# Kernel optimization log

Measured on AMD Instinct MI355X. Metric: run time of the kernel, lower is better.

The kernel has to match this reference:

```python
import jax, jax.numpy as jnp
import numpy as np
from jax.scipy.special import ndtr, logsumexp

K = 2  # top-k experts (init kwarg k=2)


def setup_inputs() -> dict:
    key = jax.random.key(0)
    k1, k2, k3, k4 = jax.random.split(key, 4)
    B, D, E = 131072, 1024, 64
    x_flat = jax.random.normal(k1, (B, D), jnp.float32)
    # Original inits w_gate/w_noise to zeros; use small random weights so
    # top-k routing is non-degenerate for correctness testing.
    w_gate = jax.random.normal(k2, (D, E), jnp.float32) * 0.02
    w_noise = jax.random.normal(k3, (D, E), jnp.float32) * 0.02
    eps = jax.random.normal(k4, (B, E), jnp.float32)  # reified torch.randn_like
    return {"x_flat": x_flat, "w_gate": w_gate, "w_noise": w_noise, "eps": eps}


def _cv_squared(v):
    # torch .var() is unbiased (ddof=1)
    return jnp.var(v, ddof=1) / (jnp.mean(v) ** 2 + 1e-10)


def reference(x_flat, w_gate, w_noise, eps):
    B = x_flat.shape[0]
    clean_logits = x_flat @ w_gate                                  # [B, E]
    noise_stddev = jax.nn.softplus(x_flat @ w_noise) + 0.01         # [B, E]
    logits = clean_logits + eps * noise_stddev                      # noisy logits (training)

    top_vals, top_idx = jax.lax.top_k(logits, K + 1)                # [B, K+1], sorted desc
    top_k_gates = jax.nn.softmax(top_vals[:, :K], axis=-1)          # [B, K]
    gates = jnp.zeros_like(logits).at[jnp.arange(B)[:, None], top_idx[:, :K]].set(top_k_gates)

    # _prob_in_top_k load estimate (noisy gating, k < num_experts, training)
    thr_if_in = top_vals[:, K:K + 1]                                # (k+1)-th largest
    thr_if_out = top_vals[:, K - 1:K]                               # k-th largest
    is_in = logits > thr_if_in
    prob_if_in = ndtr((clean_logits - thr_if_in) / noise_stddev)
    prob_if_out = ndtr((clean_logits - thr_if_out) / noise_stddev)
    load = jnp.where(is_in, prob_if_in, prob_if_out).sum(0)         # [E]

    importance = gates.sum(0)                                       # [E]
    z_loss = logsumexp(logits, axis=-1).mean()                      # log(sum(exp)).mean()
    load_balancing = _cv_squared(importance) + _cv_squared(load) + z_loss
    return gates, load, logits, load_balancing, importance
```

## Files before the change

kernel.cpp:

```cpp
#include <hip/hip_runtime.h>
#include <math.h>

#define B_ROWS 131072
#define D_DIM  1024
#define E_EXP  64
#define MARGIN 4e-3f

typedef _Float16 f16;
typedef _Float16 f16x8 __attribute__((ext_vector_type(8)));
typedef float    f32x4 __attribute__((ext_vector_type(4)));


__device__ __forceinline__ float softplus_f(float t) {
  return (t > 20.0f) ? t : log1pf(expf(t));
}
__device__ __forceinline__ float ndtr_f(float z) {
  return 0.5f * erfcf(-z * 0.70710678118654752f);
}
__device__ __forceinline__ void argmax64(float& v, int& vi) {
  #pragma unroll
  for (int off = 32; off > 0; off >>= 1) {
    float ov = __shfl_xor(v, off, 64);
    int   oi = __shfl_xor(vi, off, 64);
    if (ov > v || (ov == v && oi < vi)) { v = ov; vi = oi; }
  }
}
__device__ __forceinline__ float sum64(float v) {
  #pragma unroll
  for (int off = 32; off > 0; off >>= 1) v += __shfl_xor(v, off, 64);
  return v;
}

__device__ __forceinline__ void row_epilogue_exact(
    int row, int lane, float clean, float sd, float l,
    float* __restrict__ gates_buf, float* __restrict__ logits_buf,
    float& load_acc, float& imp_acc, float& z_acc)
{
  float v1 = l; int i1 = lane; argmax64(v1, i1);
  float v2 = (lane == i1) ? -INFINITY : l; int i2 = lane; argmax64(v2, i2);
  float v3 = (lane == i1 || lane == i2) ? -INFINITY : l; int i3 = lane; argmax64(v3, i3);
  (void)i3;
  const float e21 = expf(v2 - v1);
  const float g1  = 1.0f / (1.0f + e21);
  const float g2  = e21 * g1;
  const float gv  = (lane == i1) ? g1 : ((lane == i2) ? g2 : 0.0f);
  gates_buf [(size_t)row * E_EXP + lane] = gv;
  logits_buf[(size_t)row * E_EXP + lane] = l;
  const float ssum = sum64(expf(l - v1));
  z_acc += v1 + logf(ssum);
  const float thr = (l > v3) ? v3 : v2;
  load_acc += ndtr_f((clean - thr) / sd);
  imp_acc  += gv;
}


__global__ __launch_bounds__(256) void prep_wt(
    const float* __restrict__ wg, const float* __restrict__ wn, f16* __restrict__ wt,
    float* load_o, float* imp_o, float* zsum, int* flagcnt) {
  if (blockIdx.x == 0) {
    const int t = threadIdx.x;
    if (t < 64) { load_o[t] = 0.0f; imp_o[t] = 0.0f; }
    if (t == 64) zsum[0] = 0.0f;
    if (t == 65) flagcnt[0] = 0;
  }
  __shared__ float tile[64][65];
  const int m  = blockIdx.x >> 4;
  const int kt = blockIdx.x & 15;
  const int k0 = kt * 64;
  const float* src = m ? wn : wg;
  const int c = threadIdx.x & 63;
  const int r0 = threadIdx.x >> 6;
  #pragma unroll
  for (int r = r0; r < 64; r += 4)
    tile[r][c] = src[(size_t)(k0 + r) * 64 + c];
  __syncthreads();
  const int j = threadIdx.x & 63;
  #pragma unroll
  for (int col = r0; col < 64; col += 4)
    wt[(size_t)(m * 64 + col) * 1024 + k0 + j] = (f16)tile[j][col];
}

__global__ __launch_bounds__(256, 2) void gemm_fused(
    const float* __restrict__ x, const f16* __restrict__ wt,
    const float* __restrict__ eps,
    float* __restrict__ gates_buf, float* __restrict__ logits_buf,
    float* __restrict__ load_o, float* __restrict__ imp_o, float* __restrict__ zsum,
    int* __restrict__ flagcnt, int* __restrict__ flaglist)
{
  __shared__ float red[520];

  const int tid  = threadIdx.x;
  const int lane = tid & 63;
  const int wid  = tid >> 6;
  const int l15  = lane & 15;
  const int l4   = lane >> 4;
  const size_t rowbase = (size_t)blockIdx.x * 128 + wid * 32;

  const f16* wb = wt + (size_t)l15 * 1024 + l4 * 8;

  const float* xp0 = x + (rowbase +  0 + l15) * D_DIM + l4 * 8;
  const float* xp1 = x + (rowbase + 16 + l15) * D_DIM + l4 * 8;

  f32x4 acc[2][8];
  #pragma unroll
  for (int rt = 0; rt < 2; ++rt)
    #pragma unroll
    for (int et = 0; et < 8; ++et) acc[rt][et] = (f32x4)0.0f;

  float4 xa[8];
#define LOAD_A(kc) do {                                                  \
    _Pragma("unroll")                                                    \
    for (int kl = 0; kl < 2; ++kl) {                                     \
      xa[kl*4 + 0] = *(const float4*)(xp0 + (kc)*64 + kl*32 + 0);        \
      xa[kl*4 + 1] = *(const float4*)(xp0 + (kc)*64 + kl*32 + 4);        \
      xa[kl*4 + 2] = *(const float4*)(xp1 + (kc)*64 + kl*32 + 0);        \
      xa[kl*4 + 3] = *(const float4*)(xp1 + (kc)*64 + kl*32 + 4);        \
    }                                                                    \
  } while (0)

  LOAD_A(0);

  #pragma unroll 1
  for (int kc = 0; kc < 16; ++kc) {
    f16x8 b[8][2];
    #pragma unroll
    for (int et = 0; et < 8; ++et) {
      #pragma unroll
      for (int kl = 0; kl < 2; ++kl)
        b[et][kl] = *(const f16x8*)(wb + (size_t)et * 16384 + kc * 64 + kl * 32);
    }

    f16x8 af[2][2];
    #pragma unroll
    for (int kl = 0; kl < 2; ++kl)
      #pragma unroll
      for (int rt = 0; rt < 2; ++rt) {
        #pragma unroll
        for (int h = 0; h < 2; ++h) {
          const float4 v = xa[kl*4 + rt*2 + h];
          af[kl][rt][h*4 + 0] = (f16)v.x;
          af[kl][rt][h*4 + 1] = (f16)v.y;
          af[kl][rt][h*4 + 2] = (f16)v.z;
          af[kl][rt][h*4 + 3] = (f16)v.w;
        }
      }

    if (kc < 15) LOAD_A(kc + 1);

    #pragma unroll
    for (int kl = 0; kl < 2; ++kl) {
      #pragma unroll
      for (int et = 0; et < 8; ++et) {
        acc[0][et] = __builtin_amdgcn_mfma_f32_16x16x32_f16(af[kl][0], b[et][kl], acc[0][et], 0, 0, 0);
        acc[1][et] = __builtin_amdgcn_mfma_f32_16x16x32_f16(af[kl][1], b[et][kl], acc[1][et], 0, 0, 0);
      }
    }
  }
#undef LOAD_A

  float load_acc[4] = {0.f, 0.f, 0.f, 0.f};
  float imp_acc[4]  = {0.f, 0.f, 0.f, 0.f};
  float z_acc = 0.f;

  #pragma unroll
  for (int rt = 0; rt < 2; ++rt) {
    #pragma unroll
    for (int rg = 0; rg < 4; ++rg) {
      const size_t row = rowbase + rt * 16 + l4 * 4 + rg;
      float cl[4], sd[4], lg[4];
      #pragma unroll
      for (int j = 0; j < 4; ++j) {
        cl[j] = acc[rt][j][rg];
        sd[j] = softplus_f(acc[rt][4 + j][rg]) + 0.01f;
        const float ev = eps[row * E_EXP + j * 16 + l15];
        lg[j] = fmaf(ev, sd[j], cl[j]);
      }
      float v = lg[0]; int c = l15;
      #pragma unroll
      for (int j = 1; j < 4; ++j) {
        const int cj = j * 16 + l15;
        if (lg[j] > v || (lg[j] == v && cj < c)) { v = lg[j]; c = cj; }
      }
      #pragma unroll
      for (int off = 1; off < 16; off <<= 1) {
        const float ov = __shfl_xor(v, off, 64);
        const int   oc = __shfl_xor(c, off, 64);
        if (ov > v || (ov == v && oc < c)) { v = ov; c = oc; }
      }
      const float v1 = v; const int i1 = c;
      v = -INFINITY; c = 1 << 30;
      #pragma unroll
      for (int j = 0; j < 4; ++j) {
        const int cj = j * 16 + l15;
        if (cj != i1 && (lg[j] > v || (lg[j] == v && cj < c))) { v = lg[j]; c = cj; }
      }
      #pragma unroll
      for (int off = 1; off < 16; off <<= 1) {
        const float ov = __shfl_xor(v, off, 64);
        const int   oc = __shfl_xor(c, off, 64);
        if (ov > v || (ov == v && oc < c)) { v = ov; c = oc; }
      }
      const float v2 = v; const int i2 = c;
      float v3 = -INFINITY;
      #pragma unroll
      for (int j = 0; j < 4; ++j) {
        const int cj = j * 16 + l15;
        if (cj != i1 && cj != i2) v3 = fmaxf(v3, lg[j]);
      }
      #pragma unroll
      for (int off = 1; off < 16; off <<= 1) v3 = fmaxf(v3, __shfl_xor(v3, off, 64));

      if (v2 - v3 >= MARGIN) {
        const float e21 = expf(v2 - v1);
        const float g1  = 1.0f / (1.0f + e21);
        const float g2  = e21 * g1;
        float s = 0.f;
        #pragma unroll
        for (int j = 0; j < 4; ++j) s += expf(lg[j] - v1);
        #pragma unroll
        for (int off = 1; off < 16; off <<= 1) s += __shfl_xor(s, off, 64);
        if (l15 == 0) z_acc += v1 + logf(s);
        #pragma unroll
        for (int j = 0; j < 4; ++j) {
          const int cj = j * 16 + l15;
          const float gv = (cj == i1) ? g1 : ((cj == i2) ? g2 : 0.0f);
          gates_buf [row * E_EXP + cj] = gv;
          logits_buf[row * E_EXP + cj] = lg[j];
          imp_acc[j] += gv;
          const float thr = (lg[j] > v3) ? v3 : v2;
          load_acc[j] += ndtr_f((cl[j] - thr) / sd[j]);
        }
      } else {
        if (l15 == 0) { const int idx = atomicAdd(flagcnt, 1); flaglist[idx] = (int)row; }
      }
    }
  }

  #pragma unroll
  for (int j = 0; j < 4; ++j) {
    float L = load_acc[j]; L += __shfl_xor(L, 16, 64); L += __shfl_xor(L, 32, 64);
    float I = imp_acc[j];  I += __shfl_xor(I, 16, 64); I += __shfl_xor(I, 32, 64);
    if (l4 == 0) {
      red[wid * 64 + j * 16 + l15]       = L;
      red[256 + wid * 64 + j * 16 + l15] = I;
    }
  }
  {
    const float zw = sum64(z_acc);
    if (lane == 0) red[512 + wid] = zw;
  }
  __syncthreads();
  if (wid == 0) {
    const float L = red[lane] + red[64 + lane] + red[128 + lane] + red[192 + lane];
    const float I = red[256 + lane] + red[320 + lane] + red[384 + lane] + red[448 + lane];
    atomicAdd(&load_o[lane], L);
    atomicAdd(&imp_o[lane],  I);
    if (lane == 0) atomicAdd(zsum, red[512] + red[513] + red[514] + red[515]);
  }
}

__global__ __launch_bounds__(256) void fixup_k(
    const float* __restrict__ x, const float* __restrict__ wg, const float* __restrict__ wn,
    const float* __restrict__ eps,
    float* __restrict__ gates_buf, float* __restrict__ logits_buf,
    float* __restrict__ load_o, float* __restrict__ imp_o, float* __restrict__ zsum,
    const int* __restrict__ flagcnt, const int* __restrict__ flaglist)
{
  const int lane = threadIdx.x & 63;
  const int wid  = threadIdx.x >> 6;
  __shared__ float redg[4][4][64], redn[4][4][64];

  const int nf = *flagcnt;

  for (int it = blockIdx.x * 4; it < nf; it += gridDim.x * 4) {
    const int nr = (nf - it < 4) ? (nf - it) : 4;
    int rows[4];
    #pragma unroll
    for (int rr = 0; rr < 4; ++rr) rows[rr] = flaglist[it + ((rr < nr) ? rr : 0)];

    float dg[4] = {0.f,0.f,0.f,0.f}, dn[4] = {0.f,0.f,0.f,0.f};
    const int dbase = wid * 256;
    for (int d = 0; d < 256; d += 4) {
      const int db = (dbase + d) * E_EXP + lane;
      const float wgv0 = wg[db], wgv1 = wg[db + 64], wgv2 = wg[db + 128], wgv3 = wg[db + 192];
      const float wnv0 = wn[db], wnv1 = wn[db + 64], wnv2 = wn[db + 128], wnv3 = wn[db + 192];
      #pragma unroll
      for (int rr = 0; rr < 4; ++rr) {
        const float4 xv = *(const float4*)(x + (size_t)rows[rr] * D_DIM + dbase + d);
        dg[rr] = fmaf(xv.x, wgv0, dg[rr]);  dn[rr] = fmaf(xv.x, wnv0, dn[rr]);
        dg[rr] = fmaf(xv.y, wgv1, dg[rr]);  dn[rr] = fmaf(xv.y, wnv1, dn[rr]);
        dg[rr] = fmaf(xv.z, wgv2, dg[rr]);  dn[rr] = fmaf(xv.z, wnv2, dn[rr]);
        dg[rr] = fmaf(xv.w, wgv3, dg[rr]);  dn[rr] = fmaf(xv.w, wnv3, dn[rr]);
      }
    }
    #pragma unroll
    for (int rr = 0; rr < 4; ++rr) { redg[wid][rr][lane] = dg[rr]; redn[wid][rr][lane] = dn[rr]; }
    __syncthreads();
    if (wid < nr) {
      const int row = rows[wid];
      const float clean = redg[0][wid][lane] + redg[1][wid][lane] + redg[2][wid][lane] + redg[3][wid][lane];
      const float sdraw = redn[0][wid][lane] + redn[1][wid][lane] + redn[2][wid][lane] + redn[3][wid][lane];
      const float sd = softplus_f(sdraw) + 0.01f;
      const float ev = eps[(size_t)row * E_EXP + lane];
      const float l  = fmaf(ev, sd, clean);
      float la = 0.f, ia = 0.f, za = 0.f;
      row_epilogue_exact(row, lane, clean, sd, l, gates_buf, logits_buf, la, ia, za);
      atomicAdd(&load_o[lane], la);
      atomicAdd(&imp_o[lane],  ia);
      if (lane == 0) atomicAdd(zsum, za);
    }
    __syncthreads();
  }
}

__global__ void finalize_k(const float* __restrict__ load_o,
                           const float* __restrict__ imp_o,
                           const float* __restrict__ zsum,
                           float* __restrict__ out_lb) {
  const int e = threadIdx.x & 63;
  const double a = (double)load_o[e];
  const double b = (double)imp_o[e];
  double sl = a, sl2 = a * a, si = b, si2 = b * b;
  #pragma unroll
  for (int off = 32; off > 0; off >>= 1) {
    sl  += __shfl_xor(sl,  off, 64);
    sl2 += __shfl_xor(sl2, off, 64);
    si  += __shfl_xor(si,  off, 64);
    si2 += __shfl_xor(si2, off, 64);
  }
  if (e == 0) {
    const double n  = (double)E_EXP;
    const double ml = sl / n, mi = si / n;
    const double varl = (sl2 - n * ml * ml) / (n - 1.0);
    const double vari = (si2 - n * mi * mi) / (n - 1.0);
    const double cvl = varl / (ml * ml + 1e-10);
    const double cvi = vari / (mi * mi + 1e-10);
    const double z  = (double)zsum[0] / (double)B_ROWS;
    out_lb[0] = (float)(cvi + cvl + z);
  }
}


extern "C" void kernel_launch(void* const* d_in, const int* in_sizes, int n_in,
                              void* d_out, int out_size, void* d_ws, size_t ws_size,
                              hipStream_t stream) {
  const float* x   = (const float*)d_in[0];
  const float* wg  = (const float*)d_in[1];
  const float* wn  = (const float*)d_in[2];
  const float* eps = (const float*)d_in[3];

  float* out    = (float*)d_out;
  float* gates  = out;
  float* load_o = out + (size_t)B_ROWS * E_EXP;
  float* logits = load_o + E_EXP;
  float* lb     = logits + (size_t)B_ROWS * E_EXP;
  float* imp    = lb + 1;

  float* zsum     = (float*)d_ws;
  int*   flagcnt  = (int*)d_ws + 2;
  int*   flaglist = (int*)((char*)d_ws + 256);
  f16*   wt       = (f16*)((char*)d_ws + 256 + 4 * (size_t)B_ROWS);

  prep_wt<<<32, 256, 0, stream>>>(wg, wn, wt, load_o, imp, zsum, flagcnt);
  gemm_fused<<<B_ROWS / 128, 256, 0, stream>>>(
      x, wt, eps, gates, logits, load_o, imp, zsum, flagcnt, flaglist);
  fixup_k<<<512, 256, 0, stream>>>(x, wg, wn, eps, gates, logits, load_o, imp, zsum, flagcnt, flaglist);
  finalize_k<<<1, 64, 0, stream>>>(load_o, imp, zsum, lb);
}
```

Measured before the change: 311.0 us.

## Halve rows per wave in fused gating GEMM to raise occupancy

Each wave now computes 16 rows instead of 32, so the block covers 64 rows and the grid doubles. Accumulator and A-fragment registers are halved, and launch bounds are raised to allow 4 blocks per CU, aiming for more latency hiding on the memory-bound x stream. The cost is that each weight (B) fragment loaded from global/L2 is reused for only one row tile, doubling weight traffic per row.

```diff
diff --git a/kernel.cpp b/kernel.cpp
--- a/kernel.cpp
+++ b/kernel.cpp
@@ -80,7 +80,7 @@
     wt[(size_t)(m * 64 + col) * 1024 + k0 + j] = (f16)tile[j][col];
 }
 
-__global__ __launch_bounds__(256, 2) void gemm_fused(
+__global__ __launch_bounds__(256, 4) void gemm_fused(
     const float* __restrict__ x, const f16* __restrict__ wt,
     const float* __restrict__ eps,
     float* __restrict__ gates_buf, float* __restrict__ logits_buf,
@@ -94,67 +94,55 @@
   const int wid  = tid >> 6;
   const int l15  = lane & 15;
   const int l4   = lane >> 4;
-  const size_t rowbase = (size_t)blockIdx.x * 128 + wid * 32;
+  const size_t rowbase = ((size_t)blockIdx.x * 4 + wid) * 16;
 
   const f16* wb = wt + (size_t)l15 * 1024 + l4 * 8;
-
-  const float* xp0 = x + (rowbase +  0 + l15) * D_DIM + l4 * 8;
-  const float* xp1 = x + (rowbase + 16 + l15) * D_DIM + l4 * 8;
-
-  f32x4 acc[2][8];
-  #pragma unroll
-  for (int rt = 0; rt < 2; ++rt)
-    #pragma unroll
-    for (int et = 0; et < 8; ++et) acc[rt][et] = (f32x4)0.0f;
-
-  float4 xa[8];
+  const float* xp = x + (rowbase + l15) * D_DIM + l4 * 8;
+
+  f32x4 acc[8];
+  #pragma unroll
+  for (int et = 0; et < 8; ++et) acc[et] = (f32x4)0.0f;
+
+  float4 xa[4];
 #define LOAD_A(kc) do {                                                  \
-    _Pragma("unroll")                                                    \
-    for (int kl = 0; kl < 2; ++kl) {                                     \
-      xa[kl*4 + 0] = *(const float4*)(xp0 + (kc)*64 + kl*32 + 0);        \
-      xa[kl*4 + 1] = *(const float4*)(xp0 + (kc)*64 + kl*32 + 4);        \
-      xa[kl*4 + 2] = *(const float4*)(xp1 + (kc)*64 + kl*32 + 0);        \
-      xa[kl*4 + 3] = *(const float4*)(xp1 + (kc)*64 + kl*32 + 4);        \
-    }                                                                    \
+    xa[0] = *(const float4*)(xp + (kc)*64 +  0);                         \
+    xa[1] = *(const float4*)(xp + (kc)*64 +  4);                         \
+    xa[2] = *(const float4*)(xp + (kc)*64 + 32);                         \
+    xa[3] = *(const float4*)(xp + (kc)*64 + 36);                         \
   } while (0)
 
   LOAD_A(0);
 
   #pragma unroll 1
   for (int kc = 0; kc < 16; ++kc) {
-    f16x8 b[8][2];
-    #pragma unroll
-    for (int et = 0; et < 8; ++et) {
-      #pragma unroll
-      for (int kl = 0; kl < 2; ++kl)
-        b[et][kl] = *(const f16x8*)(wb + (size_t)et * 16384 + kc * 64 + kl * 32);
-    }
-
-    f16x8 af[2][2];
+    f16x8 b0[8], b1[8];
+    #pragma unroll
+    for (int et = 0; et < 8; ++et)
+      b0[et] = *(const f16x8*)(wb + (size_t)et * 16384 + kc * 64);
+    #pragma unroll
+    for (int et = 0; et < 8; ++et)
+      b1[et] = *(const f16x8*)(wb + (size_t)et * 16384 + kc * 64 + 32);
+
+    f16x8 af[2];
     #pragma unroll
     for (int kl = 0; kl < 2; ++kl)
       #pragma unroll
-      for (int rt = 0; rt < 2; ++rt) {
-        #pragma unroll
-        for (int h = 0; h < 2; ++h) {
-          const float4 v = xa[kl*4 + rt*2 + h];
-          af[kl][rt][h*4 + 0] = (f16)v.x;
-          af[kl][rt][h*4 + 1] = (f16)v.y;
-          af[kl][rt][h*4 + 2] = (f16)v.z;
-          af[kl][rt][h*4 + 3] = (f16)v.w;
-        }
+      for (int h = 0; h < 2; ++h) {
+        const float4 v = xa[kl*2 + h];
+        af[kl][h*4 + 0] = (f16)v.x;
+        af[kl][h*4 + 1] = (f16)v.y;
+        af[kl][h*4 + 2] = (f16)v.z;
+        af[kl][h*4 + 3] = (f16)v.w;
       }
 
     if (kc < 15) LOAD_A(kc + 1);
 
     #pragma unroll
-    for (int kl = 0; kl < 2; ++kl) {
-      #pragma unroll
-      for (int et = 0; et < 8; ++et) {
-        acc[0][et] = __builtin_amdgcn_mfma_f32_16x16x32_f16(af[kl][0], b[et][kl], acc[0][et], 0, 0, 0);
-        acc[1][et] = __builtin_amdgcn_mfma_f32_16x16x32_f16(af[kl][1], b[et][kl], acc[1][et], 0, 0, 0);
-      }
-    }
+    for (int et = 0; et < 8; ++et)
+      acc[et] = __builtin_amdgcn_mfma_f32_16x16x32_f16(af[0], b0[et], acc[et], 0, 0, 0);
+    #pragma unroll
+    for (int et = 0; et < 8; ++et)
+      acc[et] = __builtin_amdgcn_mfma_f32_16x16x32_f16(af[1], b1[et], acc[et], 0, 0, 0);
   }
 #undef LOAD_A
 
@@ -163,76 +151,73 @@
   float z_acc = 0.f;
 
   #pragma unroll
-  for (int rt = 0; rt < 2; ++rt) {
-    #pragma unroll
-    for (int rg = 0; rg < 4; ++rg) {
-      const size_t row = rowbase + rt * 16 + l4 * 4 + rg;
-      float cl[4], sd[4], lg[4];
-      #pragma unroll
-      for (int j = 0; j < 4; ++j) {
-        cl[j] = acc[rt][j][rg];
-        sd[j] = softplus_f(acc[rt][4 + j][rg]) + 0.01f;
-        const float ev = eps[row * E_EXP + j * 16 + l15];
-        lg[j] = fmaf(ev, sd[j], cl[j]);
-      }
-      float v = lg[0]; int c = l15;
-      #pragma unroll
-      for (int j = 1; j < 4; ++j) {
-        const int cj = j * 16 + l15;
-        if (lg[j] > v || (lg[j] == v && cj < c)) { v = lg[j]; c = cj; }
-      }
-      #pragma unroll
-      for (int off = 1; off < 16; off <<= 1) {
-        const float ov = __shfl_xor(v, off, 64);
-        const int   oc = __shfl_xor(c, off, 64);
-        if (ov > v || (ov == v && oc < c)) { v = ov; c = oc; }
-      }
-      const float v1 = v; const int i1 = c;
-      v = -INFINITY; c = 1 << 30;
+  for (int rg = 0; rg < 4; ++rg) {
+    const size_t row = rowbase + l4 * 4 + rg;
+    float cl[4], sd[4], lg[4];
+    #pragma unroll
+    for (int j = 0; j < 4; ++j) {
+      cl[j] = acc[j][rg];
+      sd[j] = softplus_f(acc[4 + j][rg]) + 0.01f;
+      const float ev = eps[row * E_EXP + j * 16 + l15];
+      lg[j] = fmaf(ev, sd[j], cl[j]);
+    }
+    float v = lg[0]; int c = l15;
+    #pragma unroll
+    for (int j = 1; j < 4; ++j) {
+      const int cj = j * 16 + l15;
+      if (lg[j] > v || (lg[j] == v && cj < c)) { v = lg[j]; c = cj; }
+    }
+    #pragma unroll
+    for (int off = 1; off < 16; off <<= 1) {
+      const float ov = __shfl_xor(v, off, 64);
+      const int   oc = __shfl_xor(c, off, 64);
+      if (ov > v || (ov == v && oc < c)) { v = ov; c = oc; }
+    }
+    const float v1 = v; const int i1 = c;
+    v = -INFINITY; c = 1 << 30;
+    #pragma unroll
+    for (int j = 0; j < 4; ++j) {
+      const int cj = j * 16 + l15;
+      if (cj != i1 && (lg[j] > v || (lg[j] == v && cj < c))) { v = lg[j]; c = cj; }
+    }
+    #pragma unroll
+    for (int off = 1; off < 16; off <<= 1) {
+      const float ov = __shfl_xor(v, off, 64);
+      const int   oc = __shfl_xor(c, off, 64);
+      if (ov > v || (ov == v && oc < c)) { v = ov; c = oc; }
+    }
+    const float v2 = v; const int i2 = c;
+    float v3 = -INFINITY;
+    #pragma unroll
+    for (int j = 0; j < 4; ++j) {
+      const int cj = j * 16 + l15;
+      if (cj != i1 && cj != i2) v3 = fmaxf(v3, lg[j]);
+    }
+    #pragma unroll
+    for (int off = 1; off < 16; off <<= 1) v3 = fmaxf(v3, __shfl_xor(v3, off, 64));
+
+    if (v2 - v3 >= MARGIN) {
+      const float e21 = expf(v2 - v1);
+      const float g1  = 1.0f / (1.0f + e21);
+      const float g2  = e21 * g1;
+      float s = 0.f;
+      #pragma unroll
+      for (int j = 0; j < 4; ++j) s += expf(lg[j] - v1);
+      #pragma unroll
+      for (int off = 1; off < 16; off <<= 1) s += __shfl_xor(s, off, 64);
+      if (l15 == 0) z_acc += v1 + logf(s);
       #pragma unroll
       for (int j = 0; j < 4; ++j) {
         const int cj = j * 16 + l15;
-        if (cj != i1 && (lg[j] > v || (lg[j] == v && cj < c))) { v = lg[j]; c = cj; }
+        const float gv = (cj == i1) ? g1 : ((cj == i2) ? g2 : 0.0f);
+        gates_buf [row * E_EXP + cj] = gv;
+        logits_buf[row * E_EXP + cj] = lg[j];
+        imp_acc[j] += gv;
+        const float thr = (lg[j] > v3) ? v3 : v2;
+        load_acc[j] += ndtr_f((cl[j] - thr) / sd[j]);
       }
-      #pragma unroll
-      for (int off = 1; off < 16; off <<= 1) {
-        const float ov = __shfl_xor(v, off, 64);
-        const int   oc = __shfl_xor(c, off, 64);
-        if (ov > v || (ov == v && oc < c)) { v = ov; c = oc; }
-      }
-      const float v2 = v; const int i2 = c;
-      float v3 = -INFINITY;
-      #pragma unroll
-      for (int j = 0; j < 4; ++j) {
-        const int cj = j * 16 + l15;
-        if (cj != i1 && cj != i2) v3 = fmaxf(v3, lg[j]);
-      }
-      #pragma unroll
-      for (int off = 1; off < 16; off <<= 1) v3 = fmaxf(v3, __shfl_xor(v3, off, 64));
-
-      if (v2 - v3 >= MARGIN) {
-        const float e21 = expf(v2 - v1);
-        const float g1  = 1.0f / (1.0f + e21);
-        const float g2  = e21 * g1;
-        float s = 0.f;
-        #pragma unroll
-        for (int j = 0; j < 4; ++j) s += expf(lg[j] - v1);
-        #pragma unroll
-        for (int off = 1; off < 16; off <<= 1) s += __shfl_xor(s, off, 64);
-        if (l15 == 0) z_acc += v1 + logf(s);
-        #pragma unroll
-        for (int j = 0; j < 4; ++j) {
-          const int cj = j * 16 + l15;
-          const float gv = (cj == i1) ? g1 : ((cj == i2) ? g2 : 0.0f);
-          gates_buf [row * E_EXP + cj] = gv;
-          logits_buf[row * E_EXP + cj] = lg[j];
-          imp_acc[j] += gv;
-          const float thr = (lg[j] > v3) ? v3 : v2;
-          load_acc[j] += ndtr_f((cl[j] - thr) / sd[j]);
-        }
-      } else {
-        if (l15 == 0) { const int idx = atomicAdd(flagcnt, 1); flaglist[idx] = (int)row; }
-      }
+    } else {
+      if (l15 == 0) { const int idx = atomicAdd(flagcnt, 1); flaglist[idx] = (int)row; }
     }
   }
 
@@ -362,7 +347,7 @@
   f16*   wt       = (f16*)((char*)d_ws + 256 + 4 * (size_t)B_ROWS);
 
   prep_wt<<<32, 256, 0, stream>>>(wg, wn, wt, load_o, imp, zsum, flagcnt);
-  gemm_fused<<<B_ROWS / 128, 256, 0, stream>>>(
+  gemm_fused<<<B_ROWS / 64, 256, 0, stream>>>(
       x, wt, eps, gates, logits, load_o, imp, zsum, flagcnt, flaglist);
   fixup_k<<<512, 256, 0, stream>>>(x, wg, wn, eps, gates, logits, load_o, imp, zsum, flagcnt, flaglist);
   finalize_k<<<1, 64, 0, stream>>>(load_o, imp, zsum, lb);
```

Result: slower. 411.2 us (+32.2%).
